# Kernel tuning notes

Measured on AMD Instinct MI355X. Metric: run time of the kernel, lower is better.

Reference implementation:

```python
import jax, jax.numpy as jnp
import numpy as np

N_NODE = 50000
D_FEAT = 128
N_EDGE = 625000
SIM_THRESH = 0.1


def setup_inputs() -> dict:
    key = jax.random.key(0)
    k1, k2, k3, k4, k5 = jax.random.split(key, 5)
    features = jax.random.normal(k1, (N_NODE, D_FEAT), dtype=jnp.float32)
    edge_weight = jax.random.uniform(k2, (N_EDGE,), dtype=jnp.float32)
    gate = jax.random.uniform(k3, (1,), dtype=jnp.float32)
    row = jax.random.randint(k4, (N_EDGE,), 0, N_NODE)
    col = jax.random.randint(k5, (N_EDGE,), 0, N_NODE)
    # avoid self-loops so the original's att[0,0]==0 / diagonal-removal branches
    # behave as the common (no self-loop) path
    col = jnp.where(col == row, (col + 1) % N_NODE, col)
    edge_index = jnp.stack([row, col], axis=0).astype(jnp.int64)
    return {"edge_index": edge_index, "edge_weight": edge_weight,
            "features": features, "gate": gate}


def reference(edge_index, edge_weight, features, gate):
    n_node = features.shape[0]
    row, col = edge_index[0], edge_index[1]
    # per-edge cosine similarity via normalized feature gather
    nrm = jnp.maximum(jnp.linalg.norm(features, axis=1, keepdims=True), 1e-12)
    fn = features / nrm
    sim = jnp.sum(fn[row] * fn[col], axis=1)            # [E]
    sim = jnp.where(sim < SIM_THRESH, 0.0, sim)         # threshold (all remaining >= 0.1)
    # row-wise L1 normalize over the sparse adjacency
    row_sum = jax.ops.segment_sum(jnp.abs(sim), row, num_segments=n_node)  # [N]
    denom = jnp.where(row_sum > 0, row_sum, 1.0)
    sim_norm = sim / denom[row]
    # degree-based self-loop weight lam = 1/(deg+1); only affects diagonal edges
    degree = jax.ops.segment_sum((sim_norm != 0).astype(sim_norm.dtype), row,
                                 num_segments=n_node)
    lam = 1.0 / (degree + 1.0)
    att_edge = sim_norm + jnp.where(row == col, lam[row], 0.0)
    att_edge = jnp.exp(att_edge)
    # learnable gate blend + clamp
    out = gate[0] * edge_weight + (1.0 - gate[0]) * att_edge
    return jnp.maximum(out, 0.0)
```

## Files before the change

### kernel.cpp

```cpp
#include <hip/hip_runtime.h>
#include <hip/hip_fp16.h>
#include <math.h>

#define N_NODE 50000
#define D_FEAT 128
#define N_EDGE 625000
#define SIM_THRESH 0.1f
#define SCREEN_LO 0.08f
#define BAND_EPS 5e-4f

typedef float v2f __attribute__((ext_vector_type(2)));

__global__ void prep_kernel(const float* __restrict__ feat,
                            float* __restrict__ inv_nrm,
                            __half* __restrict__ fn16,
                            unsigned int* __restrict__ fp8tab,
                            float* __restrict__ row_sum,
                            float* __restrict__ degree) {
    int g = blockIdx.x * blockDim.x + threadIdx.x;
    if (g < N_NODE) { row_sum[g] = 0.0f; degree[g] = 0.0f; }
    int node = g >> 5;
    int lane = g & 31;
    if (node >= N_NODE) return;
    float4 v = ((const float4*)(feat + (size_t)node * D_FEAT))[lane];
    float ss = v.x * v.x + v.y * v.y + v.z * v.z + v.w * v.w;
#pragma unroll
    for (int o = 16; o > 0; o >>= 1) ss += __shfl_down(ss, o, 32);
    ss = __shfl(ss, 0, 32);
    float inv = 1.0f / fmaxf(sqrtf(ss), 1e-12f);
    if (lane == 0) inv_nrm[node] = inv;
    float x0 = v.x * inv, x1 = v.y * inv, x2 = v.z * inv, x3 = v.w * inv;
    __half2 h0 = __floats2half2_rn(x0, x1);
    __half2 h1 = __floats2half2_rn(x2, x3);
    uint2 p;
    p.x = *(unsigned int*)&h0;
    p.y = *(unsigned int*)&h1;
    ((uint2*)(fn16 + (size_t)node * D_FEAT))[lane] = p;
    int w = __builtin_amdgcn_cvt_pk_fp8_f32(x0, x1, 0, false);
    w = __builtin_amdgcn_cvt_pk_fp8_f32(x2, x3, w, true);
    fp8tab[(size_t)node * 32 + lane] = (unsigned int)w;
}

__global__ __launch_bounds__(256)
void edge_sim8_kernel(const int* __restrict__ row,
                      const int* __restrict__ col,
                      const float* __restrict__ feat,
                      const float* __restrict__ inv_nrm,
                      const __half* __restrict__ fn16,
                      const unsigned int* __restrict__ fp8tab,
                      float* __restrict__ sim_out,
                      float* __restrict__ row_sum,
                      float* __restrict__ degree) {
    int g = blockIdx.x * blockDim.x + threadIdx.x;
    int edge = g >> 3;
    int lane = g & 7;
    if (edge >= N_EDGE) return;
    int r = row[edge];
    int c = col[edge];

    uint4 aw = ((const uint4*)(fp8tab + (size_t)r * 32))[lane];
    uint4 bw = ((const uint4*)(fp8tab + (size_t)c * 32))[lane];
    float d = 0.0f;
    {
        const unsigned int* awp = (const unsigned int*)&aw;
        const unsigned int* bwp = (const unsigned int*)&bw;
#pragma unroll
        for (int i = 0; i < 4; i++) {
            v2f alo = __builtin_amdgcn_cvt_pk_f32_fp8((int)awp[i], false);
            v2f ahi = __builtin_amdgcn_cvt_pk_f32_fp8((int)awp[i], true);
            v2f blo = __builtin_amdgcn_cvt_pk_f32_fp8((int)bwp[i], false);
            v2f bhi = __builtin_amdgcn_cvt_pk_f32_fp8((int)bwp[i], true);
            d = fmaf(alo.x, blo.x, d); d = fmaf(alo.y, blo.y, d);
            d = fmaf(ahi.x, bhi.x, d); d = fmaf(ahi.y, bhi.y, d);
        }
    }
#pragma unroll
    for (int o = 4; o > 0; o >>= 1) d += __shfl_down(d, o, 8);
    d = __shfl(d, 0, 8);

    float s = 0.0f;
    if (d > SCREEN_LO) {
        const float4* ar = (const float4*)(fn16 + (size_t)r * D_FEAT);
        const float4* br = (const float4*)(fn16 + (size_t)c * D_FEAT);
        float4 a0 = ar[lane], a1 = ar[lane + 8];
        float4 b0 = br[lane], b1 = br[lane + 8];
        const __half2* ah0 = (const __half2*)&a0;
        const __half2* bh0 = (const __half2*)&b0;
        const __half2* ah1 = (const __half2*)&a1;
        const __half2* bh1 = (const __half2*)&b1;
        float dh = 0.0f;
#pragma unroll
        for (int i = 0; i < 4; i++) {
            float2 afv = __half22float2(ah0[i]);
            float2 bfv = __half22float2(bh0[i]);
            dh = fmaf(afv.x, bfv.x, dh);
            dh = fmaf(afv.y, bfv.y, dh);
            float2 afw = __half22float2(ah1[i]);
            float2 bfw = __half22float2(bh1[i]);
            dh = fmaf(afw.x, bfw.x, dh);
            dh = fmaf(afw.y, bfw.y, dh);
        }
#pragma unroll
        for (int o = 4; o > 0; o >>= 1) dh += __shfl_down(dh, o, 8);
        dh = __shfl(dh, 0, 8);
        if (fabsf(dh - SIM_THRESH) < BAND_EPS) {
            const float4* fr = (const float4*)(feat + (size_t)r * D_FEAT);
            const float4* fc = (const float4*)(feat + (size_t)c * D_FEAT);
            float dd = 0.0f;
#pragma unroll
            for (int q = 0; q < 4; q++) {
                float4 av = fr[lane + q * 8];
                float4 bv = fc[lane + q * 8];
                dd += av.x * bv.x + av.y * bv.y + av.z * bv.z + av.w * bv.w;
            }
#pragma unroll
            for (int o = 4; o > 0; o >>= 1) dd += __shfl_down(dd, o, 8);
            dd = __shfl(dd, 0, 8);
            dh = dd * inv_nrm[r] * inv_nrm[c];
        }
        s = (dh < SIM_THRESH) ? 0.0f : dh;
    }
    if (lane == 0) {
        sim_out[edge] = s;
        if (s != 0.0f) {
            atomicAdd(&row_sum[r], s);
            atomicAdd(&degree[r], 1.0f);
        }
    }
}

__global__ void edge_out_kernel(const int* __restrict__ row,
                                const int* __restrict__ col,
                                const float* __restrict__ sim,
                                const float* __restrict__ row_sum,
                                const float* __restrict__ degree,
                                const float* __restrict__ ew,
                                const float* __restrict__ gate,
                                float* __restrict__ out) {
    int e = blockIdx.x * blockDim.x + threadIdx.x;
    if (e >= N_EDGE) return;
    int r = row[e];
    float rs = row_sum[r];
    float denom = (rs > 0.0f) ? rs : 1.0f;
    float att = sim[e] / denom;
    if (r == col[e]) att += 1.0f / (degree[r] + 1.0f);
    att = expf(att);
    float gv = gate[0];
    float o = gv * ew[e] + (1.0f - gv) * att;
    out[e] = fmaxf(o, 0.0f);
}

__global__ void inv_norm_kernel(const float* __restrict__ feat,
                                float* __restrict__ inv_nrm,
                                float* __restrict__ row_sum,
                                float* __restrict__ degree) {
    int g = blockIdx.x * blockDim.x + threadIdx.x;
    if (g < N_NODE) { row_sum[g] = 0.0f; degree[g] = 0.0f; }
    int node = g >> 5;
    int lane = g & 31;
    if (node >= N_NODE) return;
    float4 v = ((const float4*)(feat + (size_t)node * D_FEAT))[lane];
    float ss = v.x * v.x + v.y * v.y + v.z * v.z + v.w * v.w;
#pragma unroll
    for (int o = 16; o > 0; o >>= 1) ss += __shfl_down(ss, o, 32);
    if (lane == 0) inv_nrm[node] = 1.0f / fmaxf(sqrtf(ss), 1e-12f);
}

__global__ void edge_sim_kernel(const int* __restrict__ row,
                                const int* __restrict__ col,
                                const float* __restrict__ feat,
                                const float* __restrict__ inv_nrm,
                                float* __restrict__ sim_out,
                                float* __restrict__ row_sum,
                                float* __restrict__ degree) {
    int g = blockIdx.x * blockDim.x + threadIdx.x;
    int edge = g >> 5;
    int lane = g & 31;
    if (edge >= N_EDGE) return;
    int r = row[edge];
    int c = col[edge];
    float4 a = ((const float4*)(feat + (size_t)r * D_FEAT))[lane];
    float4 b = ((const float4*)(feat + (size_t)c * D_FEAT))[lane];
    float d = a.x * b.x + a.y * b.y + a.z * b.z + a.w * b.w;
#pragma unroll
    for (int o = 16; o > 0; o >>= 1) d += __shfl_down(d, o, 32);
    if (lane == 0) {
        float s = d * inv_nrm[r] * inv_nrm[c];
        if (s < SIM_THRESH) s = 0.0f;
        sim_out[edge] = s;
        if (s != 0.0f) {
            atomicAdd(&row_sum[r], s);
            atomicAdd(&degree[r], 1.0f);
        }
    }
}

extern "C" void kernel_launch(void* const* d_in, const int* in_sizes, int n_in,
                              void* d_out, int out_size, void* d_ws, size_t ws_size,
                              hipStream_t stream) {
    const int*   edge_index = (const int*)d_in[0];
    const float* ew         = (const float*)d_in[1];
    const float* feat       = (const float*)d_in[2];
    const float* gate       = (const float*)d_in[3];
    float*       out        = (float*)d_out;

    const int* row = edge_index;
    const int* col = edge_index + N_EDGE;

    float* row_sum = (float*)d_ws;
    float* degree  = row_sum + N_NODE;
    float* inv_nrm = degree + N_NODE;
    float* sim     = inv_nrm + N_NODE;
    __half* fn16   = (__half*)(sim + N_EDGE);
    unsigned int* fp8tab = (unsigned int*)(fn16 + (size_t)N_NODE * D_FEAT);

    size_t need = (size_t)(3 * N_NODE + N_EDGE) * 4
                + (size_t)N_NODE * D_FEAT * 2
                + (size_t)N_NODE * D_FEAT;

    const int block = 256;

    if (ws_size >= need) {
        {
            long long threads = (long long)N_NODE * 32;
            prep_kernel<<<(int)((threads + block - 1) / block), block, 0, stream>>>(
                feat, inv_nrm, fn16, fp8tab, row_sum, degree);
        }
        {
            long long threads = (long long)N_EDGE * 8;
            edge_sim8_kernel<<<(int)((threads + block - 1) / block), block, 0, stream>>>(
                row, col, feat, inv_nrm, fn16, fp8tab, sim, row_sum, degree);
        }
        edge_out_kernel<<<(N_EDGE + block - 1) / block, block, 0, stream>>>(
            row, col, sim, row_sum, degree, ew, gate, out);
    } else {
        {
            long long threads = (long long)N_NODE * 32;
            inv_norm_kernel<<<(int)((threads + block - 1) / block), block, 0, stream>>>(
                feat, inv_nrm, row_sum, degree);
        }
        {
            long long threads = (long long)N_EDGE * 32;
            edge_sim_kernel<<<(int)((threads + block - 1) / block), block, 0, stream>>>(
                row, col, feat, inv_nrm, sim, row_sum, degree);
        }
        edge_out_kernel<<<(N_EDGE + block - 1) / block, block, 0, stream>>>(
            row, col, sim, row_sum, degree, ew, gate, out);
    }
}
```

Baseline: 127.0 us.

## Use int8 sdot4 screening, fdot2 fp16 dot, xor shuffles, vectorized output kernel

Replaces the fp8 screening table with symmetric int8 quantization so the coarse dot product uses sdot4 integer dot instructions, and uses the fdot2 instruction for the fp16 refinement. Butterfly xor shuffles replace shuffle-down plus broadcast, and row/col indices are loaded nontemporally. The output kernel now handles four edges per thread with vector nontemporal loads and stores. Int8 quantization changes screening accuracy against the 0.08 screen threshold, so the margin may need to hold for correctness.

```diff
diff --git a/kernel.cpp b/kernel.cpp
--- a/kernel.cpp
+++ b/kernel.cpp
@@ -10,11 +10,26 @@
 #define BAND_EPS 5e-4f
 
 typedef float v2f __attribute__((ext_vector_type(2)));
+typedef int   v4i __attribute__((ext_vector_type(4)));
+typedef float v4f __attribute__((ext_vector_type(4)));
+
+#if __has_builtin(__builtin_amdgcn_sdot4)
+#define USE_SDOT4 1
+#else
+#define USE_SDOT4 0
+#endif
+
+#if __has_builtin(__builtin_amdgcn_fdot2)
+#define USE_FDOT2 1
+typedef _Float16 h2v __attribute__((ext_vector_type(2)));
+#else
+#define USE_FDOT2 0
+#endif
 
 __global__ void prep_kernel(const float* __restrict__ feat,
                             float* __restrict__ inv_nrm,
                             __half* __restrict__ fn16,
-                            unsigned int* __restrict__ fp8tab,
+                            unsigned int* __restrict__ qtab,
                             float* __restrict__ row_sum,
                             float* __restrict__ degree) {
     int g = blockIdx.x * blockDim.x + threadIdx.x;
@@ -25,8 +40,7 @@
     float4 v = ((const float4*)(feat + (size_t)node * D_FEAT))[lane];
     float ss = v.x * v.x + v.y * v.y + v.z * v.z + v.w * v.w;
 #pragma unroll
-    for (int o = 16; o > 0; o >>= 1) ss += __shfl_down(ss, o, 32);
-    ss = __shfl(ss, 0, 32);
+    for (int o = 16; o > 0; o >>= 1) ss += __shfl_xor(ss, o, 32);
     float inv = 1.0f / fmaxf(sqrtf(ss), 1e-12f);
     if (lane == 0) inv_nrm[node] = inv;
     float x0 = v.x * inv, x1 = v.y * inv, x2 = v.z * inv, x3 = v.w * inv;
@@ -36,9 +50,19 @@
     p.x = *(unsigned int*)&h0;
     p.y = *(unsigned int*)&h1;
     ((uint2*)(fn16 + (size_t)node * D_FEAT))[lane] = p;
-    int w = __builtin_amdgcn_cvt_pk_fp8_f32(x0, x1, 0, false);
-    w = __builtin_amdgcn_cvt_pk_fp8_f32(x2, x3, w, true);
-    fp8tab[(size_t)node * 32 + lane] = (unsigned int)w;
+#if USE_SDOT4
+    int q0 = (int)rintf(x0 * 127.0f);
+    int q1 = (int)rintf(x1 * 127.0f);
+    int q2 = (int)rintf(x2 * 127.0f);
+    int q3 = (int)rintf(x3 * 127.0f);
+    unsigned int w = (unsigned int)(q0 & 0xff) | ((unsigned int)(q1 & 0xff) << 8) |
+                     ((unsigned int)(q2 & 0xff) << 16) | ((unsigned int)(q3 & 0xff) << 24);
+#else
+    int wi = __builtin_amdgcn_cvt_pk_fp8_f32(x0, x1, 0, false);
+    wi = __builtin_amdgcn_cvt_pk_fp8_f32(x2, x3, wi, true);
+    unsigned int w = (unsigned int)wi;
+#endif
+    qtab[(size_t)node * 32 + lane] = w;
 }
 
 __global__ __launch_bounds__(256)
@@ -47,7 +71,7 @@
                       const float* __restrict__ feat,
                       const float* __restrict__ inv_nrm,
                       const __half* __restrict__ fn16,
-                      const unsigned int* __restrict__ fp8tab,
+                      const unsigned int* __restrict__ qtab,
                       float* __restrict__ sim_out,
                       float* __restrict__ row_sum,
                       float* __restrict__ degree) {
@@ -55,15 +79,29 @@
     int edge = g >> 3;
     int lane = g & 7;
     if (edge >= N_EDGE) return;
-    int r = row[edge];
-    int c = col[edge];
-
-    uint4 aw = ((const uint4*)(fp8tab + (size_t)r * 32))[lane];
-    uint4 bw = ((const uint4*)(fp8tab + (size_t)c * 32))[lane];
-    float d = 0.0f;
+    int r = __builtin_nontemporal_load(row + edge);
+    int c = __builtin_nontemporal_load(col + edge);
+
+    uint4 aw = ((const uint4*)(qtab + (size_t)r * 32))[lane];
+    uint4 bw = ((const uint4*)(qtab + (size_t)c * 32))[lane];
+    float d;
+#if USE_SDOT4
     {
         const unsigned int* awp = (const unsigned int*)&aw;
         const unsigned int* bwp = (const unsigned int*)&bw;
+        int acc = 0;
+#pragma unroll
+        for (int i = 0; i < 4; i++)
+            acc = __builtin_amdgcn_sdot4((int)awp[i], (int)bwp[i], acc, false);
+#pragma unroll
+        for (int o = 4; o > 0; o >>= 1) acc += __shfl_xor(acc, o, 8);
+        d = (float)acc * (1.0f / 16129.0f);
+    }
+#else
+    {
+        const unsigned int* awp = (const unsigned int*)&aw;
+        const unsigned int* bwp = (const unsigned int*)&bw;
+        d = 0.0f;
 #pragma unroll
         for (int i = 0; i < 4; i++) {
             v2f alo = __builtin_amdgcn_cvt_pk_f32_fp8((int)awp[i], false);
@@ -73,10 +111,10 @@
             d = fmaf(alo.x, blo.x, d); d = fmaf(alo.y, blo.y, d);
             d = fmaf(ahi.x, bhi.x, d); d = fmaf(ahi.y, bhi.y, d);
         }
-    }
-#pragma unroll
-    for (int o = 4; o > 0; o >>= 1) d += __shfl_down(d, o, 8);
-    d = __shfl(d, 0, 8);
+#pragma unroll
+        for (int o = 4; o > 0; o >>= 1) d += __shfl_xor(d, o, 8);
+    }
+#endif
 
     float s = 0.0f;
     if (d > SCREEN_LO) {
@@ -84,25 +122,40 @@
         const float4* br = (const float4*)(fn16 + (size_t)c * D_FEAT);
         float4 a0 = ar[lane], a1 = ar[lane + 8];
         float4 b0 = br[lane], b1 = br[lane + 8];
-        const __half2* ah0 = (const __half2*)&a0;
-        const __half2* bh0 = (const __half2*)&b0;
-        const __half2* ah1 = (const __half2*)&a1;
-        const __half2* bh1 = (const __half2*)&b1;
         float dh = 0.0f;
-#pragma unroll
-        for (int i = 0; i < 4; i++) {
-            float2 afv = __half22float2(ah0[i]);
-            float2 bfv = __half22float2(bh0[i]);
-            dh = fmaf(afv.x, bfv.x, dh);
-            dh = fmaf(afv.y, bfv.y, dh);
-            float2 afw = __half22float2(ah1[i]);
-            float2 bfw = __half22float2(bh1[i]);
-            dh = fmaf(afw.x, bfw.x, dh);
-            dh = fmaf(afw.y, bfw.y, dh);
-        }
-#pragma unroll
-        for (int o = 4; o > 0; o >>= 1) dh += __shfl_down(dh, o, 8);
-        dh = __shfl(dh, 0, 8);
+#if USE_FDOT2
+        {
+            const h2v* ah0 = (const h2v*)&a0;
+            const h2v* bh0 = (const h2v*)&b0;
+            const h2v* ah1 = (const h2v*)&a1;
+            const h2v* bh1 = (const h2v*)&b1;
+#pragma unroll
+            for (int i = 0; i < 4; i++) {
+                dh = __builtin_amdgcn_fdot2(ah0[i], bh0[i], dh, false);
+                dh = __builtin_amdgcn_fdot2(ah1[i], bh1[i], dh, false);
+            }
+        }
+#else
+        {
+            const __half2* ah0 = (const __half2*)&a0;
+            const __half2* bh0 = (const __half2*)&b0;
+            const __half2* ah1 = (const __half2*)&a1;
+            const __half2* bh1 = (const __half2*)&b1;
+#pragma unroll
+            for (int i = 0; i < 4; i++) {
+                float2 afv = __half22float2(ah0[i]);
+                float2 bfv = __half22float2(bh0[i]);
+                dh = fmaf(afv.x, bfv.x, dh);
+                dh = fmaf(afv.y, bfv.y, dh);
+                float2 afw = __half22float2(ah1[i]);
+                float2 bfw = __half22float2(bh1[i]);
+                dh = fmaf(afw.x, bfw.x, dh);
+                dh = fmaf(afw.y, bfw.y, dh);
+            }
+        }
+#endif
+#pragma unroll
+        for (int o = 4; o > 0; o >>= 1) dh += __shfl_xor(dh, o, 8);
         if (fabsf(dh - SIM_THRESH) < BAND_EPS) {
             const float4* fr = (const float4*)(feat + (size_t)r * D_FEAT);
             const float4* fc = (const float4*)(feat + (size_t)c * D_FEAT);
@@ -114,8 +167,7 @@
                 dd += av.x * bv.x + av.y * bv.y + av.z * bv.z + av.w * bv.w;
             }
 #pragma unroll
-            for (int o = 4; o > 0; o >>= 1) dd += __shfl_down(dd, o, 8);
-            dd = __shfl(dd, 0, 8);
+            for (int o = 4; o > 0; o >>= 1) dd += __shfl_xor(dd, o, 8);
             dh = dd * inv_nrm[r] * inv_nrm[c];
         }
         s = (dh < SIM_THRESH) ? 0.0f : dh;
@@ -137,17 +189,24 @@
                                 const float* __restrict__ ew,
                                 const float* __restrict__ gate,
                                 float* __restrict__ out) {
-    int e = blockIdx.x * blockDim.x + threadIdx.x;
-    if (e >= N_EDGE) return;
-    int r = row[e];
-    float rs = row_sum[r];
-    float denom = (rs > 0.0f) ? rs : 1.0f;
-    float att = sim[e] / denom;
-    if (r == col[e]) att += 1.0f / (degree[r] + 1.0f);
-    att = expf(att);
+    int t = blockIdx.x * blockDim.x + threadIdx.x;
+    if (t >= N_EDGE / 4) return;
+    v4i r4 = __builtin_nontemporal_load((const v4i*)row + t);
+    v4i c4 = __builtin_nontemporal_load((const v4i*)col + t);
+    v4f s4 = __builtin_nontemporal_load((const v4f*)sim + t);
+    v4f w4 = __builtin_nontemporal_load((const v4f*)ew + t);
     float gv = gate[0];
-    float o = gv * ew[e] + (1.0f - gv) * att;
-    out[e] = fmaxf(o, 0.0f);
+    float og = 1.0f - gv;
+    v4f o4;
+#pragma unroll
+    for (int i = 0; i < 4; i++) {
+        int   ri = r4[i];
+        float rs = row_sum[ri];
+        float att = s4[i] / ((rs > 0.0f) ? rs : 1.0f);
+        if (ri == c4[i]) att += 1.0f / (degree[ri] + 1.0f);
+        o4[i] = fmaxf(gv * w4[i] + og * expf(att), 0.0f);
+    }
+    __builtin_nontemporal_store(o4, (v4f*)out + t);
 }
 
 __global__ void inv_norm_kernel(const float* __restrict__ feat,
@@ -212,7 +271,7 @@
     float* inv_nrm = degree + N_NODE;
     float* sim     = inv_nrm + N_NODE;
     __half* fn16   = (__half*)(sim + N_EDGE);
-    unsigned int* fp8tab = (unsigned int*)(fn16 + (size_t)N_NODE * D_FEAT);
+    unsigned int* qtab = (unsigned int*)(fn16 + (size_t)N_NODE * D_FEAT);
 
     size_t need = (size_t)(3 * N_NODE + N_EDGE) * 4
                 + (size_t)N_NODE * D_FEAT * 2
@@ -224,15 +283,18 @@
         {
             long long threads = (long long)N_NODE * 32;
             prep_kernel<<<(int)((threads + block - 1) / block), block, 0, stream>>>(
-                feat, inv_nrm, fn16, fp8tab, row_sum, degree);
+                feat, inv_nrm, fn16, qtab, row_sum, degree);
         }
         {
             long long threads = (long long)N_EDGE * 8;
             edge_sim8_kernel<<<(int)((threads + block - 1) / block), block, 0, stream>>>(
-                row, col, feat, inv_nrm, fn16, fp8tab, sim, row_sum, degree);
-        }
-        edge_out_kernel<<<(N_EDGE + block - 1) / block, block, 0, stream>>>(
-            row, col, sim, row_sum, degree, ew, gate, out);
+                row, col, feat, inv_nrm, fn16, qtab, sim, row_sum, degree);
+        }
+        {
+            int threads = N_EDGE / 4;
+            edge_out_kernel<<<(threads + block - 1) / block, block, 0, stream>>>(
+                row, col, sim, row_sum, degree, ew, gate, out);
+        }
     } else {
         {
             long long threads = (long long)N_NODE * 32;
@@ -244,7 +306,10 @@
             edge_sim_kernel<<<(int)((threads + block - 1) / block), block, 0, stream>>>(
                 row, col, feat, inv_nrm, sim, row_sum, degree);
         }
-        edge_out_kernel<<<(N_EDGE + block - 1) / block, block, 0, stream>>>(
-            row, col, sim, row_sum, degree, ew, gate, out);
-    }
-}
+        {
+            int threads = N_EDGE / 4;
+            edge_out_kernel<<<(threads + block - 1) / block, block, 0, stream>>>(
+                row, col, sim, row_sum, degree, ew, gate, out);
+        }
+    }
+}
```

After: 127.3 us. About the same (+0.2%).
